# Kernel tuning notes

Hardware: AMD Instinct MI355X
Metric: run time of the kernel (lower is better)

The kernel has to match this reference:

```python
import jax, jax.numpy as jnp
import numpy as np

BN_EPS = 1e-5


def setup_inputs() -> dict:
    key = jax.random.key(0)
    ks = jax.random.split(key, 3)
    B, S, C, H, W = 4, 8, 64, 96, 96
    P = 6
    DIM = 768
    x = jax.random.normal(ks[0], (B, S, C, H, W), dtype=jnp.float32)
    conv_w = jax.random.normal(ks[1], (C, C, 3, 3), dtype=jnp.float32) * 0.05
    conv_b = jnp.zeros((C,), dtype=jnp.float32)
    bn_gamma = jnp.ones((C,), dtype=jnp.float32)
    bn_beta = jnp.zeros((C,), dtype=jnp.float32)
    bn_mean = jnp.zeros((C,), dtype=jnp.float32)
    bn_var = jnp.ones((C,), dtype=jnp.float32)
    proj_w = jax.random.normal(ks[2], (DIM, P * P * C), dtype=jnp.float32) * 0.02
    proj_b = jnp.zeros((DIM,), dtype=jnp.float32)
    mask = jnp.ones((P, P), dtype=jnp.float32)
    return {"x": x, "conv_w": conv_w, "conv_b": conv_b,
            "bn_gamma": bn_gamma, "bn_beta": bn_beta,
            "bn_mean": bn_mean, "bn_var": bn_var,
            "proj_w": proj_w, "proj_b": proj_b,
            "mask": mask, "patch_size": P}


def reference(x, conv_w, conv_b, bn_gamma, bn_beta, bn_mean, bn_var,
              proj_w, proj_b, mask, patch_size):
    B, S, C, H, W = x.shape
    p = patch_size
    Cout = conv_w.shape[0]
    # Fuse the per-frame loop: run conv over all B*S frames at once.
    xf = x.reshape(B * S, C, H, W)
    y = jax.lax.conv_general_dilated(
        xf, conv_w, window_strides=(1, 1), padding=[(1, 1), (1, 1)],
        dimension_numbers=("NCHW", "OIHW", "NCHW"))
    y = y + conv_b[None, :, None, None]
    # BatchNorm2d (eval-mode running stats); Dropout2d is identity at eval.
    inv = jax.lax.rsqrt(bn_var + BN_EPS)
    y = (y - bn_mean[None, :, None, None]) * (bn_gamma * inv)[None, :, None, None] \
        + bn_beta[None, :, None, None]
    y = jax.nn.gelu(y, approximate=False)  # torch GELU default = exact erf
    y = y.reshape(B, S, Cout, H, W)
    # Patch extraction, row-major over (l_idx, r_idx) exactly as the loop.
    pr = H // p  # patches per row
    patches = y.reshape(B, S, Cout, pr, p, pr, p).transpose(0, 1, 3, 5, 2, 4, 6)
    patches = patches.reshape(B, S, pr * pr, Cout, p, p) * mask  # [B,S,P,C,p,p]
    # Flatten(start_dim=2 on [B,S,C,p,p]) + Linear + GELU, batched over patches.
    flat = patches.reshape(B, S, pr * pr, Cout * p * p)
    tokens = jax.nn.gelu(
        jnp.einsum("bsnf,df->bsnd", flat, proj_w) + proj_b, approximate=False)
    return tokens, patches
```

## Files before the change

kernel.cpp:

```cpp
#include <hip/hip_runtime.h>
#include <hip/hip_bf16.h>
#include <math.h>


typedef unsigned short u16;
typedef __bf16 bf16x8 __attribute__((ext_vector_type(8)));
typedef float f32x4 __attribute__((ext_vector_type(4)));

#define NFRM 32
#define CH 64
#define HW 96
#define HWP 98
#define KP 2304
#define DIMN 768
#define MTOK 8192
#define TOKN (MTOK * DIMN)
#define NPAT (MTOK * KP)
#define XHWC_ELEMS ((size_t)NFRM * HWP * HWP * CH)
#define BP_OFF XHWC_ELEMS
#define PW_OFF (BP_OFF + 36864)
#define ABF_OFF (PW_OFF + 1769472)
#define WS_NEED_FUSED (((size_t)ABF_OFF + (size_t)NPAT) * 2)
#define BSTR 200

static __device__ __forceinline__ u16 f2b(float f) {
  unsigned u = __builtin_bit_cast(unsigned, f);
  u += 0x7fffu + ((u >> 16) & 1u);
  return (u16)(u >> 16);
}
static __device__ __forceinline__ float gelu_f(float x) {
  return 0.5f * x * (1.0f + erff(x * 0.7071067811865476f));
}

typedef __attribute__((address_space(3))) unsigned int lds_uint;
typedef __attribute__((address_space(1))) const unsigned int g_uint;
static __device__ __forceinline__ void gload16(const u16* g, u16* s) {
  __builtin_amdgcn_global_load_lds((g_uint*)g, (lds_uint*)s, 16, 0, 0);
}

__global__ __launch_bounds__(256) void k_halo(u16* __restrict__ xhwc) {
  const int e = blockIdx.x * 256 + threadIdx.x;
  const int g = e & 7;
  const int rest = e >> 3;
  const int p = rest % 388, f = rest / 388;
  int r, c;
  if (p < 98)       { r = 0;       c = p; }
  else if (p < 196) { r = 97;      c = p - 98; }
  else if (p < 292) { r = p - 195; c = 0; }
  else              { r = p - 291; c = 97; }
  *(uint4*)&xhwc[(((size_t)f * HWP + r) * HWP + c) * CH + g * 8] = (uint4){0, 0, 0, 0};
}

__global__ __launch_bounds__(256) void k_transpose(const float* __restrict__ x,
                                                   u16* __restrict__ xhwc) {
  __shared__ u16 tile[96 * 66];
  const int f = blockIdx.x / 96, h = blockIdx.x % 96;
  const int t = threadIdx.x;
  const float* xp = x + (size_t)f * CH * HW * HW + (size_t)h * HW;
#pragma unroll
  for (int k = 0; k < 6; ++k) {
    int e = (k * 256 + t) * 4;
    int ci = e / 96, w = e % 96;
    float4 v = *(const float4*)(xp + (size_t)ci * (HW * HW) + w);
    tile[(w + 0) * 66 + ci] = f2b(v.x);
    tile[(w + 1) * 66 + ci] = f2b(v.y);
    tile[(w + 2) * 66 + ci] = f2b(v.z);
    tile[(w + 3) * 66 + ci] = f2b(v.w);
  }
  __syncthreads();
  u16* op = xhwc + ((size_t)(f * HWP + h + 1) * HWP + 1) * CH;
#pragma unroll
  for (int k = 0; k < 12; ++k) {
    int e2 = (k * 256 + t) * 2;
    int w = e2 >> 6, ci = e2 & 63;
    *(unsigned*)(op + e2) = *(const unsigned*)(&tile[w * 66 + ci]);
  }
}

__global__ __launch_bounds__(256) void k_bpack(const float* __restrict__ w,
                                               u16* __restrict__ bp) {
  int e = blockIdx.x * 256 + threadIdx.x;
  int co = e / 576, r = e - co * 576, tap = r >> 6, ci = r & 63;
  bp[e] = f2b(w[(co * 64 + ci) * 9 + tap]);
}

__global__ __launch_bounds__(256) void k_pw(const float* __restrict__ pw,
                                            u16* __restrict__ dst) {
  int e = (blockIdx.x * 256 + threadIdx.x) * 4;
  float4 v = *(const float4*)(pw + e);
  ushort4 o;
  o.x = f2b(v.x); o.y = f2b(v.y); o.z = f2b(v.z); o.w = f2b(v.w);
  *(ushort4*)(dst + e) = o;
}

__global__ __launch_bounds__(256, 2) void k_conv(
    const u16* __restrict__ xhwc, const u16* __restrict__ bw,
    const float* __restrict__ cb, const float* __restrict__ gma,
    const float* __restrict__ bta, const float* __restrict__ mu,
    const float* __restrict__ var, const float* __restrict__ msk,
    float* __restrict__ pout, u16* __restrict__ abf) {
  __shared__ alignas(16) char SMEM[76800];
  u16* Asm = (u16*)SMEM;
  u16* Bsm = (u16*)(SMEM + 51200);
  float* Fsm = (float*)SMEM;

  const int bx = blockIdx.x;
  const int f = bx >> 5, rem = bx & 31, pr = rem >> 1, half = rem & 1;
  const int t = threadIdx.x, wv = t >> 6, l = t & 63, quad = l >> 4, lm = l & 15;
  const int wm = wv >> 1, wn = wv & 1;

  const u16* sbase = xhwc + (((size_t)f * HWP + pr * 6) * HWP + half * 48) * CH;
  const int pc = l >> 3;
  const int gsw = (l & 7) ^ pc;
  for (int c = wv; c < 50; c += 4) {
    const int p = c * 8 + pc;
    const int row = p / 50, ac = p - row * 50;
    gload16(sbase + ((size_t)row * HWP + ac) * CH + gsw * 8, Asm + c * 512);
  }

  int pb[9];
#pragma unroll
  for (int mf = 0; mf < 9; ++mf) {
    const int i16 = wm * 9 + mf;
    pb[mf] = (i16 / 3) * 50 + (i16 % 3) * 16 + lm;
  }
  f32x4 acc[9][2];
#pragma unroll
  for (int mf = 0; mf < 9; ++mf) {
    acc[mf][0] = (f32x4){0.f, 0.f, 0.f, 0.f};
    acc[mf][1] = (f32x4){0.f, 0.f, 0.f, 0.f};
  }

#pragma unroll
  for (int ph = 0; ph < 3; ++ph) {
    if (ph > 0) __syncthreads();
    for (int e = t; e < 1536; e += 256) {
      const int co = e / 24, kk = e - co * 24;
      *(uint4*)&Bsm[co * BSTR + kk * 8] =
          *(const uint4*)&bw[co * 576 + ph * 192 + kk * 8];
    }
    __syncthreads();
#pragma unroll
    for (int tp = 0; tp < 3; ++tp) {
      const int di = ph, dj = tp;
#pragma unroll
      for (int ks = 0; ks < 2; ++ks) {
        const int kq = ks * 4 + quad;
        const bf16x8 b0 = *(const bf16x8*)&Bsm[(wn * 32 + lm) * BSTR + tp * 64 + ks * 32 + quad * 8];
        const bf16x8 b1 = *(const bf16x8*)&Bsm[(wn * 32 + 16 + lm) * BSTR + tp * 64 + ks * 32 + quad * 8];
#pragma unroll
        for (int mf = 0; mf < 9; ++mf) {
          const int p = pb[mf] + di * 50 + dj;
          const bf16x8 a = *(const bf16x8*)&Asm[p * 64 + ((kq ^ (p & 7)) << 3)];
          acc[mf][0] = __builtin_amdgcn_mfma_f32_16x16x32_bf16(a, b0, acc[mf][0], 0, 0, 0);
          acc[mf][1] = __builtin_amdgcn_mfma_f32_16x16x32_bf16(a, b1, acc[mf][1], 0, 0, 0);
        }
      }
    }
  }

  __syncthreads();
#pragma unroll
  for (int nf = 0; nf < 2; ++nf) {
    const int co = wn * 32 + nf * 16 + lm;
    const float scv = gma[co] * rsqrtf(var[co] + 1e-5f);
    const float b2v = (cb[co] - mu[co]) * scv + bta[co];
#pragma unroll
    for (int mf = 0; mf < 9; ++mf) {
#pragma unroll
      for (int rg = 0; rg < 4; ++rg) {
        const int sp = wm * 144 + mf * 16 + quad * 4 + rg;
        const int orow = sp / 48, oc = sp - orow * 48;
        const int nl = oc / 6, pj = oc - nl * 6;
        const int jj = orow * 6 + pj;
        float v = acc[mf][nf][rg] * scv + b2v;
        v = gelu_f(v) * msk[jj];
        Fsm[nl * 2304 + co * 36 + jj] = v;
      }
    }
  }
  __syncthreads();
  const size_t brow = (size_t)(f * 256 + pr * 16 + half * 8) * KP;
  float* pbase = pout + brow;
#pragma unroll
  for (int k = 0; k < 18; ++k) {
    const int li = t + k * 256;
    *(float4*)&pbase[li * 4] = *(const float4*)&Fsm[li * 4];
  }
  if (abf) {
    u16* adst = abf + brow;
#pragma unroll
    for (int k = 0; k < 18; ++k) {
      const int li = t + k * 256;
      const float4 w = *(const float4*)&Fsm[li * 4];
      ushort4 o;
      o.x = f2b(w.x); o.y = f2b(w.y); o.z = f2b(w.z); o.w = f2b(w.w);
      *(ushort4*)&adst[li * 4] = o;
    }
  }
}

__global__ __launch_bounds__(256) void k_cvt(const float* __restrict__ pat,
                                             u16* __restrict__ abf) {
  int e = (blockIdx.x * 256 + threadIdx.x) * 4;
  float4 v = *(const float4*)(pat + e);
  ushort4 o;
  o.x = f2b(v.x); o.y = f2b(v.y); o.z = f2b(v.z); o.w = f2b(v.w);
  *(ushort4*)(abf + e) = o;
}

__global__ __launch_bounds__(256) void k_gemm(const u16* __restrict__ A,
                                              const u16* __restrict__ Bt,
                                              const float* __restrict__ pb,
                                              float* __restrict__ out) {
  __shared__ alignas(16) u16 As[128 * 128];
  __shared__ alignas(16) u16 Bs[64 * 128];
  const int bid = blockIdx.x;
  const int logical = (bid & 7) * 96 + (bid >> 3);
  const int bn = logical % 12, bm = logical / 12;
  const int m0 = bm * 128, n0 = bn * 64;
  const int t = threadIdx.x, wv = t >> 6, l = t & 63, quad = l >> 4, lm = l & 15;
  const int rl = l >> 4;
  const int slot = l & 15;

  f32x4 acc[2][4];
#pragma unroll
  for (int s = 0; s < 2; ++s)
#pragma unroll
    for (int u = 0; u < 4; ++u) acc[s][u] = (f32x4){0.f, 0.f, 0.f, 0.f};

  for (int k0 = 0; k0 < KP; k0 += 128) {
    __syncthreads();
    for (int c = wv; c < 48; c += 4) {
      if (c < 32) {
        const int row = c * 4 + rl;
        const int gsw2 = slot ^ (row & 15);
        gload16(A + (size_t)(m0 + row) * KP + k0 + gsw2 * 8, As + c * 512);
      } else {
        const int row = (c - 32) * 4 + rl;
        const int gsw2 = slot ^ (row & 15);
        gload16(Bt + (size_t)(n0 + row) * KP + k0 + gsw2 * 8, Bs + (c - 32) * 512);
      }
    }
    __syncthreads();
#pragma unroll
    for (int ks = 0; ks < 4; ++ks) {
      const int gx = ((ks * 4 + quad) ^ lm) << 3;
      const bf16x8 a0 = *(const bf16x8*)&As[(wv * 32 + lm) * 128 + gx];
      const bf16x8 a1 = *(const bf16x8*)&As[(wv * 32 + 16 + lm) * 128 + gx];
#pragma unroll
      for (int u = 0; u < 4; ++u) {
        const bf16x8 b = *(const bf16x8*)&Bs[(u * 16 + lm) * 128 + gx];
        acc[0][u] = __builtin_amdgcn_mfma_f32_16x16x32_bf16(a0, b, acc[0][u], 0, 0, 0);
        acc[1][u] = __builtin_amdgcn_mfma_f32_16x16x32_bf16(a1, b, acc[1][u], 0, 0, 0);
      }
    }
  }
#pragma unroll
  for (int u = 0; u < 4; ++u) {
    const int n = n0 + u * 16 + lm;
    const float bias = pb[n];
#pragma unroll
    for (int s = 0; s < 2; ++s) {
#pragma unroll
      for (int rg = 0; rg < 4; ++rg) {
        const int m = m0 + wv * 32 + s * 16 + quad * 4 + rg;
        out[(size_t)m * DIMN + n] = gelu_f(acc[s][u][rg] + bias);
      }
    }
  }
}

extern "C" void kernel_launch(void* const* d_in, const int* in_sizes, int n_in,
                              void* d_out, int out_size, void* d_ws, size_t ws_size,
                              hipStream_t stream) {
  const float* x = (const float*)d_in[0];
  const float* conv_w = (const float*)d_in[1];
  const float* conv_b = (const float*)d_in[2];
  const float* bn_gamma = (const float*)d_in[3];
  const float* bn_beta = (const float*)d_in[4];
  const float* bn_mean = (const float*)d_in[5];
  const float* bn_var = (const float*)d_in[6];
  const float* proj_w = (const float*)d_in[7];
  const float* proj_b = (const float*)d_in[8];
  const float* mask = (const float*)d_in[9];
  float* out = (float*)d_out;
  float* patches = out + TOKN;
  u16* ws = (u16*)d_ws;
  u16* xhwc = ws;
  u16* bp = ws + BP_OFF;
  u16* pw = ws + PW_OFF;

  const bool fused = ws_size >= WS_NEED_FUSED;
  u16* abf = fused ? ws + ABF_OFF : (u16*)nullptr;

  k_halo<<<388, 256, 0, stream>>>(xhwc);
  k_transpose<<<NFRM * HW, 256, 0, stream>>>(x, xhwc);
  k_bpack<<<144, 256, 0, stream>>>(conv_w, bp);
  k_pw<<<1728, 256, 0, stream>>>(proj_w, pw);
  k_conv<<<NFRM * 32, 256, 0, stream>>>(xhwc, bp, conv_b, bn_gamma, bn_beta,
                                        bn_mean, bn_var, mask, patches, abf);
  if (!fused) {
    k_cvt<<<18432, 256, 0, stream>>>(patches, xhwc);
    abf = xhwc;
  }
  k_gemm<<<64 * 12, 256, 0, stream>>>(abf, pw, proj_b, out);
}
```

Baseline: 299.4 us.

## Fold halo zeroing into transpose, merge prep kernels, widen conv to 384 threads

```diff
diff --git a/kernel.cpp b/kernel.cpp
--- a/kernel.cpp
+++ b/kernel.cpp
@@ -38,19 +38,6 @@
   __builtin_amdgcn_global_load_lds((g_uint*)g, (lds_uint*)s, 16, 0, 0);
 }
 
-__global__ __launch_bounds__(256) void k_halo(u16* __restrict__ xhwc) {
-  const int e = blockIdx.x * 256 + threadIdx.x;
-  const int g = e & 7;
-  const int rest = e >> 3;
-  const int p = rest % 388, f = rest / 388;
-  int r, c;
-  if (p < 98)       { r = 0;       c = p; }
-  else if (p < 196) { r = 97;      c = p - 98; }
-  else if (p < 292) { r = p - 195; c = 0; }
-  else              { r = p - 291; c = 97; }
-  *(uint4*)&xhwc[(((size_t)f * HWP + r) * HWP + c) * CH + g * 8] = (uint4){0, 0, 0, 0};
-}
-
 __global__ __launch_bounds__(256) void k_transpose(const float* __restrict__ x,
                                                    u16* __restrict__ xhwc) {
   __shared__ u16 tile[96 * 66];
@@ -68,32 +55,48 @@
     tile[(w + 3) * 66 + ci] = f2b(v.w);
   }
   __syncthreads();
-  u16* op = xhwc + ((size_t)(f * HWP + h + 1) * HWP + 1) * CH;
+  u16* frm = xhwc + (size_t)f * HWP * HWP * CH;
+  u16* op = frm + ((size_t)(h + 1) * HWP + 1) * CH;
 #pragma unroll
   for (int k = 0; k < 12; ++k) {
     int e2 = (k * 256 + t) * 2;
     int w = e2 >> 6, ci = e2 & 63;
     *(unsigned*)(op + e2) = *(const unsigned*)(&tile[w * 66 + ci]);
   }
-}
-
-__global__ __launch_bounds__(256) void k_bpack(const float* __restrict__ w,
-                                               u16* __restrict__ bp) {
-  int e = blockIdx.x * 256 + threadIdx.x;
-  int co = e / 576, r = e - co * 576, tap = r >> 6, ci = r & 63;
-  bp[e] = f2b(w[(co * 64 + ci) * 9 + tap]);
-}
-
-__global__ __launch_bounds__(256) void k_pw(const float* __restrict__ pw,
-                                            u16* __restrict__ dst) {
-  int e = (blockIdx.x * 256 + threadIdx.x) * 4;
-  float4 v = *(const float4*)(pw + e);
-  ushort4 o;
-  o.x = f2b(v.x); o.y = f2b(v.y); o.z = f2b(v.z); o.w = f2b(v.w);
-  *(ushort4*)(dst + e) = o;
-}
-
-__global__ __launch_bounds__(256, 2) void k_conv(
+  const uint4 z = (uint4){0, 0, 0, 0};
+  if (t < 16) {
+    const int col = (t < 8) ? 0 : 97;
+    const int g = t & 7;
+    *(uint4*)&frm[((size_t)(h + 1) * HWP + col) * CH + g * 8] = z;
+  }
+  if (h == 0) {
+    for (int i = t; i < 784; i += 256) *(uint4*)&frm[(size_t)i * 8] = z;
+  }
+  if (h == 95) {
+    u16* r97 = frm + (size_t)97 * HWP * CH;
+    for (int i = t; i < 784; i += 256) *(uint4*)&r97[(size_t)i * 8] = z;
+  }
+}
+
+__global__ __launch_bounds__(256) void k_prep(const float* __restrict__ w,
+                                              const float* __restrict__ pwsrc,
+                                              u16* __restrict__ bp,
+                                              u16* __restrict__ pwd) {
+  const int b = blockIdx.x;
+  if (b < 144) {
+    int e = b * 256 + threadIdx.x;
+    int co = e / 576, r = e - co * 576, tap = r >> 6, ci = r & 63;
+    bp[e] = f2b(w[(co * 64 + ci) * 9 + tap]);
+  } else {
+    int e = ((b - 144) * 256 + threadIdx.x) * 4;
+    float4 v = *(const float4*)(pwsrc + e);
+    ushort4 o;
+    o.x = f2b(v.x); o.y = f2b(v.y); o.z = f2b(v.z); o.w = f2b(v.w);
+    *(ushort4*)(pwd + e) = o;
+  }
+}
+
+__global__ __launch_bounds__(384, 3) void k_conv(
     const u16* __restrict__ xhwc, const u16* __restrict__ bw,
     const float* __restrict__ cb, const float* __restrict__ gma,
     const float* __restrict__ bta, const float* __restrict__ mu,
@@ -112,21 +115,21 @@
   const u16* sbase = xhwc + (((size_t)f * HWP + pr * 6) * HWP + half * 48) * CH;
   const int pc = l >> 3;
   const int gsw = (l & 7) ^ pc;
-  for (int c = wv; c < 50; c += 4) {
+  for (int c = wv; c < 50; c += 6) {
     const int p = c * 8 + pc;
     const int row = p / 50, ac = p - row * 50;
     gload16(sbase + ((size_t)row * HWP + ac) * CH + gsw * 8, Asm + c * 512);
   }
 
-  int pb[9];
-#pragma unroll
-  for (int mf = 0; mf < 9; ++mf) {
-    const int i16 = wm * 9 + mf;
+  int pb[6];
+#pragma unroll
+  for (int mf = 0; mf < 6; ++mf) {
+    const int i16 = wm * 6 + mf;
     pb[mf] = (i16 / 3) * 50 + (i16 % 3) * 16 + lm;
   }
-  f32x4 acc[9][2];
-#pragma unroll
-  for (int mf = 0; mf < 9; ++mf) {
+  f32x4 acc[6][2];
+#pragma unroll
+  for (int mf = 0; mf < 6; ++mf) {
     acc[mf][0] = (f32x4){0.f, 0.f, 0.f, 0.f};
     acc[mf][1] = (f32x4){0.f, 0.f, 0.f, 0.f};
   }
@@ -134,7 +137,7 @@
 #pragma unroll
   for (int ph = 0; ph < 3; ++ph) {
     if (ph > 0) __syncthreads();
-    for (int e = t; e < 1536; e += 256) {
+    for (int e = t; e < 1536; e += 384) {
       const int co = e / 24, kk = e - co * 24;
       *(uint4*)&Bsm[co * BSTR + kk * 8] =
           *(const uint4*)&bw[co * 576 + ph * 192 + kk * 8];
@@ -149,7 +152,7 @@
         const bf16x8 b0 = *(const bf16x8*)&Bsm[(wn * 32 + lm) * BSTR + tp * 64 + ks * 32 + quad * 8];
         const bf16x8 b1 = *(const bf16x8*)&Bsm[(wn * 32 + 16 + lm) * BSTR + tp * 64 + ks * 32 + quad * 8];
 #pragma unroll
-        for (int mf = 0; mf < 9; ++mf) {
+        for (int mf = 0; mf < 6; ++mf) {
           const int p = pb[mf] + di * 50 + dj;
           const bf16x8 a = *(const bf16x8*)&Asm[p * 64 + ((kq ^ (p & 7)) << 3)];
           acc[mf][0] = __builtin_amdgcn_mfma_f32_16x16x32_bf16(a, b0, acc[mf][0], 0, 0, 0);
@@ -166,10 +169,10 @@
     const float scv = gma[co] * rsqrtf(var[co] + 1e-5f);
     const float b2v = (cb[co] - mu[co]) * scv + bta[co];
 #pragma unroll
-    for (int mf = 0; mf < 9; ++mf) {
+    for (int mf = 0; mf < 6; ++mf) {
 #pragma unroll
       for (int rg = 0; rg < 4; ++rg) {
-        const int sp = wm * 144 + mf * 16 + quad * 4 + rg;
+        const int sp = wm * 96 + mf * 16 + quad * 4 + rg;
         const int orow = sp / 48, oc = sp - orow * 48;
         const int nl = oc / 6, pj = oc - nl * 6;
         const int jj = orow * 6 + pj;
@@ -183,15 +186,15 @@
   const size_t brow = (size_t)(f * 256 + pr * 16 + half * 8) * KP;
   float* pbase = pout + brow;
 #pragma unroll
-  for (int k = 0; k < 18; ++k) {
-    const int li = t + k * 256;
+  for (int k = 0; k < 12; ++k) {
+    const int li = t + k * 384;
     *(float4*)&pbase[li * 4] = *(const float4*)&Fsm[li * 4];
   }
   if (abf) {
     u16* adst = abf + brow;
 #pragma unroll
-    for (int k = 0; k < 18; ++k) {
-      const int li = t + k * 256;
+    for (int k = 0; k < 12; ++k) {
+      const int li = t + k * 384;
       const float4 w = *(const float4*)&Fsm[li * 4];
       ushort4 o;
       o.x = f2b(w.x); o.y = f2b(w.y); o.z = f2b(w.z); o.w = f2b(w.w);
@@ -294,11 +297,9 @@
   const bool fused = ws_size >= WS_NEED_FUSED;
   u16* abf = fused ? ws + ABF_OFF : (u16*)nullptr;
 
-  k_halo<<<388, 256, 0, stream>>>(xhwc);
   k_transpose<<<NFRM * HW, 256, 0, stream>>>(x, xhwc);
-  k_bpack<<<144, 256, 0, stream>>>(conv_w, bp);
-  k_pw<<<1728, 256, 0, stream>>>(proj_w, pw);
-  k_conv<<<NFRM * 32, 256, 0, stream>>>(xhwc, bp, conv_b, bn_gamma, bn_beta,
+  k_prep<<<1872, 256, 0, stream>>>(conv_w, proj_w, bp, pw);
+  k_conv<<<NFRM * 32, 384, 0, stream>>>(xhwc, bp, conv_b, bn_gamma, bn_beta,
                                         bn_mean, bn_var, mask, patches, abf);
   if (!fused) {
     k_cvt<<<18432, 256, 0, stream>>>(patches, xhwc);
```

After: 314.8 us. 5.1% more time.
